# Performance work log

Hardware: AMD Instinct MI355X
Metric: run time of the kernel (lower is better)

The kernel has to match this reference:

```python
import jax, jax.numpy as jnp
import numpy as np

POOL = 16  # in_downsampling == internal_downsampling == 16


def _conv1x1(x, w, b):
    # x: [B,C,H,W], w: [O,C], b: [O] -> [B,O,H,W]
    return jnp.einsum('oc,bchw->bohw', w, x) + b[None, :, None, None]


def _maxpool(x, k):
    return jax.lax.reduce_window(x, -jnp.inf, jax.lax.max,
                                 (1, 1, k, k), (1, 1, k, k), 'VALID')


def setup_inputs() -> dict:
    key = jax.random.key(0)
    ks = jax.random.split(key, 7)
    B, C, Ci, H, W = 4, 256, 128, 256, 256
    s_in = 1.0 / np.sqrt(C)
    return {
        'x':   jax.random.normal(ks[0], (B, C, H, W), jnp.float32),
        'f_w': jax.random.normal(ks[1], (Ci, C), jnp.float32) * s_in,
        'f_b': jax.random.normal(ks[2], (Ci,), jnp.float32) * 0.01,
        'g_w': jax.random.normal(ks[3], (Ci, C), jnp.float32) * s_in,
        'g_b': jax.random.normal(ks[4], (Ci,), jnp.float32) * 0.01,
        'h_w': jax.random.normal(ks[5], (C, C), jnp.float32) * s_in,
        'h_b': jax.random.normal(ks[6], (C,), jnp.float32) * 0.01,
    }


def reference(x, f_w, f_b, g_w, g_b, h_w, h_b):
    B, C, H, W = x.shape
    # pooled query / key features: [B, Ci, h1, w1] and [B, Ci, h2, w2]
    fv = _maxpool(_conv1x1(x, f_w, f_b), POOL)
    gv = _maxpool(_conv1x1(x, g_w, g_b), POOL)
    # dots[b,i,j,k,l] = sum_c fv[b,c,i,j] * gv[b,c,k,l]  (channel dot-product)
    dots = jnp.einsum('bcij,bckl->bijkl', fv, gv)
    Bd, h1, w1, h2, w2 = dots.shape
    # exp=True path: softmax over the flattened (h2, w2) key positions
    dots = jax.nn.softmax(dots.reshape(Bd, h1, w1, h2 * w2), axis=-1)
    dots = dots.reshape(Bd, h1, w1, h2, w2)
    # pooled values: [B, C, h2, w2]
    hv = _maxpool(_conv1x1(x, h_w, h_b), POOL)
    # weighted sum over key positions -> [B, C, h1, w1]
    out = jnp.einsum('bijkl,bckl->bcij', dots, hv)
    # bilinear upsample (align_corners=False == half-pixel, matches jax resize)
    up = jax.image.resize(out, (B, C, H, W), method='bilinear')
    return up + x
```

## Files before the change

kernel.cpp:

```cpp
#include <hip/hip_runtime.h>
#include <hip/hip_fp16.h>

typedef _Float16 f16;
typedef _Float16 f16x4_t __attribute__((ext_vector_type(4)));
typedef _Float16 f16x8_t __attribute__((ext_vector_type(8)));
typedef float    f32x4_t __attribute__((ext_vector_type(4)));

#define NB  4
#define NC  256
#define NH  256
#define NW  256

__global__ __launch_bounds__(256) void k_convert_w(
    const float* __restrict__ f_w, const float* __restrict__ g_w,
    const float* __restrict__ h_w, f16* __restrict__ wf)
{
    int id = blockIdx.x * 256 + threadIdx.x;
    int cout = id >> 8;
    float v;
    if (cout < 128)       v = f_w[id];
    else if (cout < 256)  v = g_w[id - 128*256];
    else                  v = h_w[id - 256*256];
    wf[id] = (f16)v;
}

__device__ __forceinline__ void bar_lds() {
    asm volatile("s_waitcnt lgkmcnt(0)" ::: "memory");
    __builtin_amdgcn_s_barrier();
}

__global__ __launch_bounds__(1024, 4) void k_pooled_conv(
    const float* __restrict__ x, const f16* __restrict__ wf,
    const float* __restrict__ f_b, const float* __restrict__ g_b,
    const float* __restrict__ h_b,
    float* __restrict__ pooled_fg,
    float* __restrict__ pooledT_h)
{
    __shared__ __align__(16) char smem[65536];

    const int t    = threadIdx.x;
    const int wave = t >> 6;
    const int lane = t & 63;
    const int l15  = lane & 15;
    const int lg   = lane >> 4;
    const bool isfg = (wave < 8);
    const int coutbase = isfg ? wave * 32 : 256 + (wave - 8) * 32;

    f16x8_t bfrag[2][8];
    #pragma unroll
    for (int n = 0; n < 2; n++) {
        const f16* wr = wf + (coutbase + n*16 + l15) * 256 + lg*8;
        #pragma unroll
        for (int k = 0; k < 8; k++)
            bfrag[n][k] = *(const f16x8_t*)(wr + k*32);
    }
    float biasv[2];
    #pragma unroll
    for (int n = 0; n < 2; n++) {
        int c = coutbase + n*16 + l15;
        biasv[n] = (c < 128) ? f_b[c] : (c < 256) ? g_b[c - 128] : h_b[c - 256];
    }

    const int dx  = t & 15;
    const int dyl = (t >> 4) & 1;
    const int c8  = (t >> 5) * 8;
    const unsigned page = (unsigned)(dyl*8 + (c8 >> 5));
    const unsigned slot = (unsigned)(dx | (((c8 >> 3) & 3) << 4));
    const unsigned woff = (page << 10) + slot * 16u;

    const int bid   = blockIdx.x;
    const int b     = bid >> 7;
    const int wbase = (bid & 127) * 2;
    const float* xb = x + (size_t)b * (256u * 65536u);

    float vmax[2] = {-3.0e38f, -3.0e38f};

    auto loadst = [&](int gsd, float* r) {
        int win = wbase + (gsd >> 3);
        int s   = gsd & 7;
        int wi = (win >> 4) & 15, wj = win & 15;
        const float* src = xb + (size_t)c8 * 65536u
                         + (unsigned)((wi*16 + s*2 + dyl) * 256 + wj*16 + dx);
        #pragma unroll
        for (int cc = 0; cc < 8; cc++)
            r[cc] = src[(unsigned)cc * 65536u];
    };
    auto writest = [&](const float* r, int buf) {
        char* base = smem + buf * 32768;
        f16x8_t hv, lv;
        #pragma unroll
        for (int cc = 0; cc < 8; cc++) {
            float v = r[cc];
            f16 h = (f16)v;
            hv[cc] = h;
            lv[cc] = (f16)(v - (float)h);
        }
        *(f16x8_t*)(base + woff)         = hv;
        *(f16x8_t*)(base + 16384 + woff) = lv;
    };
    auto mfmast = [&](int buf) {
        const char* base = smem + buf * 32768 + lane * 16;
        #pragma unroll
        for (int m = 0; m < 2; m++) {
            f32x4_t acc0 = {0.f,0.f,0.f,0.f}, acc1 = {0.f,0.f,0.f,0.f};
            #pragma unroll
            for (int k = 0; k < 8; k++) {
                const char* p = base + ((m*8 + k) << 10);
                f16x8_t ah = *(const f16x8_t*)p;
                acc0 = __builtin_amdgcn_mfma_f32_16x16x32_f16(ah, bfrag[0][k], acc0, 0,0,0);
                acc1 = __builtin_amdgcn_mfma_f32_16x16x32_f16(ah, bfrag[1][k], acc1, 0,0,0);
                if (isfg) {
                    f16x8_t al = *(const f16x8_t*)(p + 16384);
                    acc0 = __builtin_amdgcn_mfma_f32_16x16x32_f16(al, bfrag[0][k], acc0, 0,0,0);
                    acc1 = __builtin_amdgcn_mfma_f32_16x16x32_f16(al, bfrag[1][k], acc1, 0,0,0);
                }
            }
            #pragma unroll
            for (int r = 0; r < 4; r++) {
                vmax[0] = fmaxf(vmax[0], acc0[r]);
                vmax[1] = fmaxf(vmax[1], acc1[r]);
            }
        }
    };
    auto finalize = [&](int win) {
        int wn = win & 255;
        #pragma unroll
        for (int n = 0; n < 2; n++) {
            float v = vmax[n];
            v = fmaxf(v, __shfl_xor(v, 16, 64));
            v = fmaxf(v, __shfl_xor(v, 32, 64));
            if (lane < 16) {
                float val = v + biasv[n];
                int c = coutbase + n*16 + lane;
                if (isfg) pooled_fg[((b*256 + c)  << 8) + wn] = val;
                else      pooledT_h[((b*256 + wn) << 8) + (c - 256)] = val;
            }
            vmax[n] = -3.0e38f;
        }
    };

    float rA[8], rB[8];
    loadst(0, rA);
    loadst(1, rB);
    writest(rA, 0);
    bar_lds();

    #pragma unroll 1
    for (int gs = 0; gs < 16; gs += 2) {
        if (gs + 2 < 16) loadst(gs + 2, rA);
        writest(rB, 1);
        mfmast(0);
        bar_lds();
        if (gs + 3 < 16) loadst(gs + 3, rB);
        if (gs + 2 < 16) writest(rA, 0);
        mfmast(1);
        if ((gs & 7) == 6) finalize(wbase + (gs >> 3));
        bar_lds();
    }
}

__global__ __launch_bounds__(256) void k_attn(
    const float* __restrict__ pooled_fg, const float* __restrict__ pooledT_h,
    float* __restrict__ attnout)
{
    __shared__ float red[4];
    __shared__ float p_lds[256];
    const int blk = blockIdx.x;
    const int b = blk >> 8;
    const int q = blk & 255;
    const int t = threadIdx.x;

    const float* fv = pooled_fg + ((b*256) << 8) + q;
    const float* gv = pooled_fg + ((b*256 + 128) << 8) + t;

    float s = 0.f;
    #pragma unroll 8
    for (int c = 0; c < 128; c++)
        s += fv[c << 8] * gv[c << 8];

    float m = s;
    #pragma unroll
    for (int o = 1; o < 64; o <<= 1) m = fmaxf(m, __shfl_xor(m, o, 64));
    if ((t & 63) == 0) red[t >> 6] = m;
    __syncthreads();
    m = fmaxf(fmaxf(red[0], red[1]), fmaxf(red[2], red[3]));
    __syncthreads();

    float p = expf(s - m);
    float sum = p;
    #pragma unroll
    for (int o = 1; o < 64; o <<= 1) sum += __shfl_xor(sum, o, 64);
    if ((t & 63) == 0) red[t >> 6] = sum;
    __syncthreads();
    sum = red[0] + red[1] + red[2] + red[3];
    p /= sum;
    p_lds[t] = p;
    __syncthreads();

    const float* hv = pooledT_h + (b << 16) + t;
    float acc = 0.f;
    #pragma unroll 8
    for (int k = 0; k < 256; k++)
        acc += p_lds[k] * hv[k << 8];
    attnout[((b*256 + t) << 8) + q] = acc;
}

__global__ __launch_bounds__(256) void k_upsample_add(
    const float* __restrict__ x, const float* __restrict__ attnout,
    float* __restrict__ out)
{
    __shared__ float L[256];
    const int blk = blockIdx.x;
    const int t = threadIdx.x;
    L[t] = attnout[(blk << 8) + t];
    __syncthreads();
    const float* xp = x   + (size_t)blk * 65536;
    float*       op = out + (size_t)blk * 65536;

    const int x4 = (t & 63) << 2;
    const int yo = t >> 6;
    float fxv[4]; int x0v[4], x1v[4];
    #pragma unroll
    for (int e = 0; e < 4; e++) {
        float sx  = (x4 + e + 0.5f) * 0.0625f - 0.5f;
        float x0f = floorf(sx);
        fxv[e] = sx - x0f;
        int ix0 = (int)x0f;
        x0v[e] = min(15, max(0, ix0));
        x1v[e] = min(15, max(0, ix0 + 1));
    }
    for (int it = 0; it < 64; it++) {
        int y = it*4 + yo;
        float sy  = (y + 0.5f) * 0.0625f - 0.5f;
        float y0f = floorf(sy);
        float fy  = sy - y0f;
        int iy0 = (int)y0f;
        int y0 = min(15, max(0, iy0));
        int y1 = min(15, max(0, iy0 + 1));
        const float* Ly0 = L + y0*16;
        const float* Ly1 = L + y1*16;
        float4 xin = *(const float4*)(xp + y*256 + x4);
        float o[4]; const float* xe = (const float*)&xin;
        #pragma unroll
        for (int e = 0; e < 4; e++) {
            float top = Ly0[x0v[e]] + fxv[e] * (Ly0[x1v[e]] - Ly0[x0v[e]]);
            float bot = Ly1[x0v[e]] + fxv[e] * (Ly1[x1v[e]] - Ly1[x0v[e]]);
            o[e] = top + fy * (bot - top) + xe[e];
        }
        float4 ov = make_float4(o[0], o[1], o[2], o[3]);
        *(float4*)(op + y*256 + x4) = ov;
    }
}

extern "C" void kernel_launch(void* const* d_in, const int* in_sizes, int n_in,
                              void* d_out, int out_size, void* d_ws, size_t ws_size,
                              hipStream_t stream)
{
    const float* x   = (const float*)d_in[0];
    const float* f_w = (const float*)d_in[1];
    const float* f_b = (const float*)d_in[2];
    const float* g_w = (const float*)d_in[3];
    const float* g_b = (const float*)d_in[4];
    const float* h_w = (const float*)d_in[5];
    const float* h_b = (const float*)d_in[6];
    float* out = (float*)d_out;

    char* ws = (char*)d_ws;
    f16*   wf        = (f16*)ws;
    float* pooled_fg = (float*)(ws + (256<<10));
    float* pooledT_h = (float*)(ws + (256<<10) + (1<<20));
    float* attnout   = (float*)(ws + (256<<10) + (2<<20));

    k_convert_w   <<<512, 256, 0, stream>>>(f_w, g_w, h_w, wf);
    k_pooled_conv <<<512, 1024, 0, stream>>>(x, wf, f_b, g_b, h_b, pooled_fg, pooledT_h);
    k_attn        <<<1024, 256, 0, stream>>>(pooled_fg, pooledT_h, attnout);
    k_upsample_add<<<1024, 256, 0, stream>>>(x, attnout, out);
}
```

Before: 316.6 us.

## Split pooled conv into separate fg and h blocks per pool window

The pooled 1x1-conv kernel used to run 1024-thread blocks where 8 waves computed f/g with hi+lo fp16 splitting and 8 waves computed h at plain fp16, covering two pool windows per block. Each block now has 512 threads and handles one window for either the f/g outputs or the h outputs, giving 2048 blocks and half the LDS per block. The h blocks stage only the high fp16 half and load 16 channels per thread, while the f/g blocks keep the hi/lo pair. This is meant to remove the imbalance where the h waves sat idle at barriers waiting for the heavier f/g waves, and to improve occupancy. In exchange, each x tile is now read from memory by two different blocks.

```diff
diff --git a/kernel.cpp b/kernel.cpp
--- a/kernel.cpp
+++ b/kernel.cpp
@@ -29,22 +29,28 @@
     __builtin_amdgcn_s_barrier();
 }
 
-__global__ __launch_bounds__(1024, 4) void k_pooled_conv(
+__global__ __launch_bounds__(512, 4) void k_pooled_conv(
     const float* __restrict__ x, const f16* __restrict__ wf,
     const float* __restrict__ f_b, const float* __restrict__ g_b,
     const float* __restrict__ h_b,
     float* __restrict__ pooled_fg,
     float* __restrict__ pooledT_h)
 {
-    __shared__ __align__(16) char smem[65536];
+    __shared__ __align__(16) char smem[32768];
+
+    const int bid  = blockIdx.x;
+    const int w    = ((bid >> 4) << 3) | (bid & 7);
+    const bool ish = (bid >> 3) & 1;
+    const int b    = w >> 8;
+    const int win  = w & 255;
+    const int wi   = win >> 4, wj = win & 15;
 
     const int t    = threadIdx.x;
     const int wave = t >> 6;
     const int lane = t & 63;
     const int l15  = lane & 15;
     const int lg   = lane >> 4;
-    const bool isfg = (wave < 8);
-    const int coutbase = isfg ? wave * 32 : 256 + (wave - 8) * 32;
+    const int coutbase = (ish ? 256 : 0) + wave * 32;
 
     f16x8_t bfrag[2][8];
     #pragma unroll
@@ -61,101 +67,145 @@
         biasv[n] = (c < 128) ? f_b[c] : (c < 256) ? g_b[c - 128] : h_b[c - 256];
     }
 
-    const int dx  = t & 15;
-    const int dyl = (t >> 4) & 1;
-    const int c8  = (t >> 5) * 8;
-    const unsigned page = (unsigned)(dyl*8 + (c8 >> 5));
-    const unsigned slot = (unsigned)(dx | (((c8 >> 3) & 3) << 4));
-    const unsigned woff = (page << 10) + slot * 16u;
-
-    const int bid   = blockIdx.x;
-    const int b     = bid >> 7;
-    const int wbase = (bid & 127) * 2;
     const float* xb = x + (size_t)b * (256u * 65536u);
-
+    const unsigned rowbase = (unsigned)((wi*16) * 256 + wj*16);
     float vmax[2] = {-3.0e38f, -3.0e38f};
 
-    auto loadst = [&](int gsd, float* r) {
-        int win = wbase + (gsd >> 3);
-        int s   = gsd & 7;
-        int wi = (win >> 4) & 15, wj = win & 15;
-        const float* src = xb + (size_t)c8 * 65536u
-                         + (unsigned)((wi*16 + s*2 + dyl) * 256 + wj*16 + dx);
-        #pragma unroll
-        for (int cc = 0; cc < 8; cc++)
-            r[cc] = src[(unsigned)cc * 65536u];
-    };
-    auto writest = [&](const float* r, int buf) {
-        char* base = smem + buf * 32768;
-        f16x8_t hv, lv;
-        #pragma unroll
-        for (int cc = 0; cc < 8; cc++) {
-            float v = r[cc];
-            f16 h = (f16)v;
-            hv[cc] = h;
-            lv[cc] = (f16)(v - (float)h);
-        }
-        *(f16x8_t*)(base + woff)         = hv;
-        *(f16x8_t*)(base + 16384 + woff) = lv;
-    };
-    auto mfmast = [&](int buf) {
-        const char* base = smem + buf * 32768 + lane * 16;
-        #pragma unroll
-        for (int m = 0; m < 2; m++) {
+    if (!ish) {
+        const int dx = t & 15;
+        const int c8 = (t >> 4) * 8;
+        const unsigned woff = ((unsigned)(c8 >> 5) << 10)
+                            + (unsigned)(dx | (((c8 >> 3) & 3) << 4)) * 16u;
+        auto loadst = [&](int gs, float* r) {
+            const float* src = xb + (size_t)c8 * 65536u + rowbase + (unsigned)(gs*256 + dx);
+            #pragma unroll
+            for (int cc = 0; cc < 8; cc++) r[cc] = src[(unsigned)cc * 65536u];
+        };
+        auto writest = [&](const float* r, int buf) {
+            char* base = smem + buf * 16384;
+            f16x8_t hv, lv;
+            #pragma unroll
+            for (int cc = 0; cc < 8; cc++) {
+                float v = r[cc]; f16 h = (f16)v;
+                hv[cc] = h; lv[cc] = (f16)(v - (float)h);
+            }
+            *(f16x8_t*)(base + woff)        = hv;
+            *(f16x8_t*)(base + 8192 + woff) = lv;
+        };
+        auto mfmast = [&](int buf) {
+            const char* base = smem + buf * 16384 + lane * 16;
             f32x4_t acc0 = {0.f,0.f,0.f,0.f}, acc1 = {0.f,0.f,0.f,0.f};
             #pragma unroll
             for (int k = 0; k < 8; k++) {
-                const char* p = base + ((m*8 + k) << 10);
+                const char* p = base + (k << 10);
                 f16x8_t ah = *(const f16x8_t*)p;
+                f16x8_t al = *(const f16x8_t*)(p + 8192);
                 acc0 = __builtin_amdgcn_mfma_f32_16x16x32_f16(ah, bfrag[0][k], acc0, 0,0,0);
                 acc1 = __builtin_amdgcn_mfma_f32_16x16x32_f16(ah, bfrag[1][k], acc1, 0,0,0);
-                if (isfg) {
-                    f16x8_t al = *(const f16x8_t*)(p + 16384);
-                    acc0 = __builtin_amdgcn_mfma_f32_16x16x32_f16(al, bfrag[0][k], acc0, 0,0,0);
-                    acc1 = __builtin_amdgcn_mfma_f32_16x16x32_f16(al, bfrag[1][k], acc1, 0,0,0);
-                }
+                acc0 = __builtin_amdgcn_mfma_f32_16x16x32_f16(al, bfrag[0][k], acc0, 0,0,0);
+                acc1 = __builtin_amdgcn_mfma_f32_16x16x32_f16(al, bfrag[1][k], acc1, 0,0,0);
             }
             #pragma unroll
             for (int r = 0; r < 4; r++) {
                 vmax[0] = fmaxf(vmax[0], acc0[r]);
                 vmax[1] = fmaxf(vmax[1], acc1[r]);
             }
-        }
-    };
-    auto finalize = [&](int win) {
-        int wn = win & 255;
+        };
+
+        float rA[8], rB[8];
+        loadst(0, rA); loadst(1, rB);
+        writest(rA, 0);
+        bar_lds();
+        #pragma unroll 1
+        for (int gs = 0; gs < 16; gs += 2) {
+            if (gs + 2 < 16) loadst(gs + 2, rA);
+            writest(rB, 1);
+            mfmast(0);
+            bar_lds();
+            if (gs + 3 < 16) loadst(gs + 3, rB);
+            if (gs + 2 < 16) writest(rA, 0);
+            mfmast(1);
+            bar_lds();
+        }
         #pragma unroll
         for (int n = 0; n < 2; n++) {
             float v = vmax[n];
             v = fmaxf(v, __shfl_xor(v, 16, 64));
             v = fmaxf(v, __shfl_xor(v, 32, 64));
             if (lane < 16) {
-                float val = v + biasv[n];
                 int c = coutbase + n*16 + lane;
-                if (isfg) pooled_fg[((b*256 + c)  << 8) + wn] = val;
-                else      pooledT_h[((b*256 + wn) << 8) + (c - 256)] = val;
-            }
-            vmax[n] = -3.0e38f;
-        }
-    };
-
-    float rA[8], rB[8];
-    loadst(0, rA);
-    loadst(1, rB);
-    writest(rA, 0);
-    bar_lds();
-
-    #pragma unroll 1
-    for (int gs = 0; gs < 16; gs += 2) {
-        if (gs + 2 < 16) loadst(gs + 2, rA);
-        writest(rB, 1);
-        mfmast(0);
+                pooled_fg[((b*256 + c) << 8) + win] = v + biasv[n];
+            }
+        }
+    } else {
+        const int dx  = t & 15;
+        const int dyl = (t >> 4) & 1;
+        const int c0  = (t >> 5) * 16;
+        const unsigned pg = (unsigned)(dyl*8 + (c0 >> 5)) << 10;
+        const unsigned w0 = pg + (unsigned)(dx | (((c0 >> 3) & 3) << 4)) * 16u;
+        const unsigned w1 = pg + (unsigned)(dx | ((((c0 + 8) >> 3) & 3) << 4)) * 16u;
+        auto loadst = [&](int gs, float* r) {
+            const float* src = xb + (size_t)c0 * 65536u + rowbase
+                             + (unsigned)((gs*2 + dyl)*256 + dx);
+            #pragma unroll
+            for (int cc = 0; cc < 16; cc++) r[cc] = src[(unsigned)cc * 65536u];
+        };
+        auto writest = [&](const float* r, int buf) {
+            char* base = smem + buf * 16384;
+            f16x8_t h0, h1;
+            #pragma unroll
+            for (int cc = 0; cc < 8; cc++) {
+                h0[cc] = (f16)r[cc];
+                h1[cc] = (f16)r[cc + 8];
+            }
+            *(f16x8_t*)(base + w0) = h0;
+            *(f16x8_t*)(base + w1) = h1;
+        };
+        auto mfmast = [&](int buf) {
+            const char* base = smem + buf * 16384 + lane * 16;
+            #pragma unroll
+            for (int m = 0; m < 2; m++) {
+                f32x4_t acc0 = {0.f,0.f,0.f,0.f}, acc1 = {0.f,0.f,0.f,0.f};
+                #pragma unroll
+                for (int k = 0; k < 8; k++) {
+                    const char* p = base + ((m*8 + k) << 10);
+                    f16x8_t ah = *(const f16x8_t*)p;
+                    acc0 = __builtin_amdgcn_mfma_f32_16x16x32_f16(ah, bfrag[0][k], acc0, 0,0,0);
+                    acc1 = __builtin_amdgcn_mfma_f32_16x16x32_f16(ah, bfrag[1][k], acc1, 0,0,0);
+                }
+                #pragma unroll
+                for (int r = 0; r < 4; r++) {
+                    vmax[0] = fmaxf(vmax[0], acc0[r]);
+                    vmax[1] = fmaxf(vmax[1], acc1[r]);
+                }
+            }
+        };
+
+        float rA[16], rB[16];
+        loadst(0, rA); loadst(1, rB);
+        writest(rA, 0);
         bar_lds();
-        if (gs + 3 < 16) loadst(gs + 3, rB);
-        if (gs + 2 < 16) writest(rA, 0);
-        mfmast(1);
-        if ((gs & 7) == 6) finalize(wbase + (gs >> 3));
-        bar_lds();
+        #pragma unroll 1
+        for (int gs = 0; gs < 8; gs += 2) {
+            if (gs + 2 < 8) loadst(gs + 2, rA);
+            writest(rB, 1);
+            mfmast(0);
+            bar_lds();
+            if (gs + 3 < 8) loadst(gs + 3, rB);
+            if (gs + 2 < 8) writest(rA, 0);
+            mfmast(1);
+            bar_lds();
+        }
+        #pragma unroll
+        for (int n = 0; n < 2; n++) {
+            float v = vmax[n];
+            v = fmaxf(v, __shfl_xor(v, 16, 64));
+            v = fmaxf(v, __shfl_xor(v, 32, 64));
+            if (lane < 16) {
+                int c = coutbase + n*16 + lane;
+                pooledT_h[((b*256 + win) << 8) + (c - 256)] = v + biasv[n];
+            }
+        }
     }
 }
 
@@ -272,7 +322,7 @@
     float* attnout   = (float*)(ws + (256<<10) + (2<<20));
 
     k_convert_w   <<<512, 256, 0, stream>>>(f_w, g_w, h_w, wf);
-    k_pooled_conv <<<512, 1024, 0, stream>>>(x, wf, f_b, g_b, h_b, pooled_fg, pooledT_h);
+    k_pooled_conv <<<2048, 512, 0, stream>>>(x, wf, f_b, g_b, h_b, pooled_fg, pooledT_h);
     k_attn        <<<1024, 256, 0, stream>>>(pooled_fg, pooledT_h, attnout);
     k_upsample_add<<<1024, 256, 0, stream>>>(x, attnout, out);
 }
```

Result: slower. 332.3 us (+5.0%).
